# Performance work log

Hardware: AMD Instinct MI355X
Metric: run time of the kernel (lower is better)

## Reference

```python
import jax, jax.numpy as jnp
import numpy as np

QMAX = 7.0            # int4 narrow range: [-7, 7]
SCALING_MIN_VAL = 2e-16


def fake_quant_weight_per_channel(w):
    """Brevitas CommonIntWeightPerChannelQuant, bit_width=4.

    Per-output-channel float scale from abs-max stats, narrow-range signed
    int4 round+clamp, then dequantize. STE so gradients pass through.
    w: [O, I, KH, KW]
    """
    amax = jnp.max(jnp.abs(w), axis=(1, 2, 3), keepdims=True)   # [O,1,1,1]
    scale = jnp.maximum(amax / QMAX, SCALING_MIN_VAL)
    wq = jnp.clip(jnp.round(w / scale), -QMAX, QMAX) * scale
    # straight-through estimator (matches Brevitas round_ste backward)
    return w + jax.lax.stop_gradient(wq - w)


def setup_inputs() -> dict:
    key = jax.random.key(0)
    kx, kw = jax.random.split(key)
    x = jax.random.normal(kx, (32, 256, 56, 56), dtype=jnp.float32)
    # conv weight [out_channels, in_channels, kh, kw]
    w = jax.random.normal(kw, (256, 256, 3, 3), dtype=jnp.float32) * 0.05
    return {"x": x, "w": w}


def reference(x, w):
    wq = fake_quant_weight_per_channel(w)
    return jax.lax.conv_general_dilated(
        x, wq,
        window_strides=(1, 1),
        padding=((1, 1), (1, 1)),
        dimension_numbers=("NCHW", "OIHW", "NCHW"),
    )
```

## Files before the change

kernel.cpp:

```cpp
#include <hip/hip_runtime.h>
#include <cstdint>
#include <cstddef>

typedef __bf16 bf16x8 __attribute__((ext_vector_type(8)));
typedef float  f32x16 __attribute__((ext_vector_type(16)));
typedef int    i32x4  __attribute__((ext_vector_type(4)));

#define QMAX 7.0f
#define SCALE_MIN 2e-16f

#define BAR()     asm volatile("s_barrier" ::: "memory")
#define WAITVM(N) asm volatile("s_waitcnt vmcnt(" #N ")" ::: "memory")

__global__ __launch_bounds__(256) void quant_w_kernel(const float* __restrict__ w,
                                                      __bf16* __restrict__ wq) {
    const int o = blockIdx.x;
    const int t = threadIdx.x;
    const float* wo = w + (size_t)o * 2304;

    float vals[9];
    float m = 0.f;
    #pragma unroll
    for (int i = 0; i < 9; ++i) {
        float v = wo[t + i * 256];
        vals[i] = v;
        m = fmaxf(m, fabsf(v));
    }
    #pragma unroll
    for (int off = 32; off >= 1; off >>= 1) m = fmaxf(m, __shfl_down(m, off));
    __shared__ float red[4];
    __shared__ float s_scale;
    if ((t & 63) == 0) red[t >> 6] = m;
    __syncthreads();
    if (t == 0) {
        float am = fmaxf(fmaxf(red[0], red[1]), fmaxf(red[2], red[3]));
        s_scale = fmaxf(am / QMAX, SCALE_MIN);
    }
    __syncthreads();
    const float scale = s_scale;

    #pragma unroll
    for (int i = 0; i < 9; ++i) {
        int idx = t + i * 256;
        int c = idx / 9;
        int tap = idx - c * 9;
        float q = rintf(vals[i] / scale);
        q = fminf(QMAX, fmaxf(-QMAX, q));
        wq[(size_t)tap * 65536 + (size_t)o * 256 + c] = (__bf16)(q * scale);
    }
}

__global__ __launch_bounds__(256) void convert_x_kernel(const float* __restrict__ x,
                                                        __bf16* __restrict__ xpad) {
    __shared__ float tile[32][33];
    const int n  = blockIdx.z;
    const int c0 = blockIdx.y * 32;
    const int p0 = blockIdx.x * 32;
    const int tx = threadIdx.x & 31;
    const int ty = threadIdx.x >> 5;

    #pragma unroll
    for (int r = 0; r < 4; ++r) {
        int c = c0 + ty + r * 8;
        tile[ty + r * 8][tx] = x[((size_t)(n * 256 + c)) * 3136 + p0 + tx];
    }
    __syncthreads();
    #pragma unroll
    for (int r = 0; r < 4; ++r) {
        int p = p0 + ty + r * 8;
        int h = p / 56, wcol = p - h * 56;
        xpad[(((size_t)n * 58 + h + 1) * 58 + (wcol + 1)) * 256 + c0 + tx] =
            (__bf16)tile[tx][ty + r * 8];
    }
}

__global__ __launch_bounds__(256) void zero_halo_kernel(__bf16* __restrict__ xpad) {
    const int t = blockIdx.x * 256 + threadIdx.x;
    const int cvec = t & 31;
    const int r    = t >> 5;
    const int n    = r / 228;
    const int pos  = r - n * 228;
    if (n >= 32) return;
    int h, wcol;
    if      (pos < 58)  { h = 0;          wcol = pos; }
    else if (pos < 116) { h = 57;         wcol = pos - 58; }
    else if (pos < 172) { h = pos - 115;  wcol = 0; }
    else                { h = pos - 171;  wcol = 57; }
    i32x4* dst = (i32x4*)(xpad + (((size_t)n * 58 + h) * 58 + wcol) * 256);
    dst[cvec] = (i32x4){0, 0, 0, 0};
}

__device__ __forceinline__ void gload_lds16(const void* g, void* l) {
    __builtin_amdgcn_global_load_lds((const __attribute__((address_space(1))) void*)g,
                                     (__attribute__((address_space(3))) void*)l,
                                     16, 0, 0);
}

__global__ __launch_bounds__(256, 2) void conv_mfma_kernel(const __bf16* __restrict__ xpad,
                                                           const __bf16* __restrict__ wq,
                                                           float* __restrict__ out) {
    extern __shared__ __align__(16) char lds[];
    const int tid  = threadIdx.x;
    const int wv   = tid >> 6;
    const int lane = tid & 63;
    const int bid  = blockIdx.x;
    const int swz  = (bid & 7) * 98 + (bid >> 3);
    const int p0   = swz * 128;

    const int wm = wv >> 1;
    const int wn = wv & 1;

    const int trow   = tid >> 2;
    const int schunk = (tid & 3) ^ ((tid >> 4) & 3);
    const __bf16* pA[4];
    #pragma unroll
    for (int j = 0; j < 4; ++j)
        pA[j] = wq + (size_t)(j * 64 + trow) * 256 + schunk * 8;
    const __bf16* pBs[2];
    #pragma unroll
    for (int j = 0; j < 2; ++j) {
        int pos = p0 + j * 64 + trow;
        int ni = pos / 3136;
        int hw = pos - ni * 3136;
        int h = hw / 56, w = hw - h * 56;
        pBs[j] = xpad + (((size_t)ni * 58 + h) * 58 + w) * 256 + schunk * 8;
    }
    const int adst = wv * 1024;
    const int bdst = 16384 + wv * 1024;

    const int l31 = lane & 31;
    const int lk  = lane >> 5;
    const int rsw = (lane >> 2) & 3;
    int kx[2];
    #pragma unroll
    for (int ks = 0; ks < 2; ++ks)
        kx[ks] = ((ks * 2 + lk) ^ rsw) * 16;
    int arow[4], brow[2];
    #pragma unroll
    for (int m = 0; m < 4; ++m) arow[m] = (wm * 128 + m * 32 + l31) * 64;
    #pragma unroll
    for (int n = 0; n < 2; ++n) brow[n] = 16384 + (wn * 64 + n * 32 + l31) * 64;

    f32x16 acc[4][2];
    #pragma unroll
    for (int m = 0; m < 4; ++m)
        #pragma unroll
        for (int n = 0; n < 2; ++n)
            acc[m][n] = (f32x16)(0.f);

    #define STAGE(STEP, BUF)                                                  \
        {                                                                     \
            const int tap_ = (STEP) >> 3, cc_ = (STEP) & 7;                   \
            const int kh_ = tap_ / 3, kw_ = tap_ - kh_ * 3;                   \
            const size_t aoff_ = (size_t)tap_ * 65536 + cc_ * 32;             \
            const size_t boff_ = (size_t)(kh_ * 58 + kw_) * 256 + cc_ * 32;   \
            gload_lds16(pA[0] + aoff_, (BUF) + adst);                         \
            gload_lds16(pA[1] + aoff_, (BUF) + adst + 4096);                  \
            gload_lds16(pA[2] + aoff_, (BUF) + adst + 8192);                  \
            gload_lds16(pA[3] + aoff_, (BUF) + adst + 12288);                 \
            gload_lds16(pBs[0] + boff_, (BUF) + bdst);                        \
            gload_lds16(pBs[1] + boff_, (BUF) + bdst + 4096);                 \
        }

    STAGE(0, lds);
    STAGE(1, lds + 24576);

    int co = 0;
    #pragma unroll 1
    for (int s = 0; s < 72; ++s) {
        if (s < 71) { WAITVM(6); } else { WAITVM(0); }
        BAR();
        int so = co + 49152; if (so >= 73728) so -= 73728;
        if (s < 70) STAGE(s + 2, lds + so);

        const char* B = lds + co;
        bf16x8 a[4][2], b[2][2];
        #pragma unroll
        for (int m = 0; m < 4; ++m)
            #pragma unroll
            for (int ks = 0; ks < 2; ++ks)
                a[m][ks] = *(const bf16x8*)(B + arow[m] + kx[ks]);
        #pragma unroll
        for (int n = 0; n < 2; ++n)
            #pragma unroll
            for (int ks = 0; ks < 2; ++ks)
                b[n][ks] = *(const bf16x8*)(B + brow[n] + kx[ks]);

        __builtin_amdgcn_s_setprio(1);
        #pragma unroll
        for (int ks = 0; ks < 2; ++ks)
            #pragma unroll
            for (int m = 0; m < 4; ++m)
                #pragma unroll
                for (int n = 0; n < 2; ++n)
                    acc[m][n] = __builtin_amdgcn_mfma_f32_32x32x16_bf16(
                        a[m][ks], b[n][ks], acc[m][n], 0, 0, 0);
        __builtin_amdgcn_s_setprio(0);

        co += 24576; if (co == 73728) co = 0;
    }
    #undef STAGE

    const int hi = lane >> 5;
    #pragma unroll
    for (int n = 0; n < 2; ++n) {
        const int pos = p0 + wn * 64 + n * 32 + l31;
        const int ni = pos / 3136;
        const int hw = pos - ni * 3136;
        float* ob = out + (size_t)ni * 802816 + hw;
        #pragma unroll
        for (int m = 0; m < 4; ++m) {
            const int om = wm * 128 + m * 32 + 4 * hi;
            #pragma unroll
            for (int r = 0; r < 16; ++r) {
                const int o = om + (r & 3) + 8 * (r >> 2);
                ob[(size_t)o * 3136] = acc[m][n][r];
            }
        }
    }
}

__global__ __launch_bounds__(256) void conv_naive_kernel(const float* __restrict__ x,
                                                         const float* __restrict__ w,
                                                         float* __restrict__ out) {
    const int n = blockIdx.z;
    const int o = blockIdx.y;
    const int strip = blockIdx.x;
    __shared__ float wqs[2304];
    __shared__ float red[4];
    __shared__ float s_scale;
    const float* wo = w + (size_t)o * 2304;
    float m = 0.f;
    for (int i = threadIdx.x; i < 2304; i += 256) m = fmaxf(m, fabsf(wo[i]));
    #pragma unroll
    for (int off = 32; off >= 1; off >>= 1) m = fmaxf(m, __shfl_down(m, off));
    if ((threadIdx.x & 63) == 0) red[threadIdx.x >> 6] = m;
    __syncthreads();
    if (threadIdx.x == 0) {
        float am = fmaxf(fmaxf(red[0], red[1]), fmaxf(red[2], red[3]));
        s_scale = fmaxf(am / QMAX, SCALE_MIN);
    }
    __syncthreads();
    const float scale = s_scale;
    for (int i = threadIdx.x; i < 2304; i += 256) {
        float q = rintf(wo[i] / scale);
        q = fminf(QMAX, fmaxf(-QMAX, q));
        wqs[i] = q * scale;
    }
    __syncthreads();
    int p = strip * 256 + threadIdx.x;
    if (p >= 3136) return;
    int h = p / 56, wcol = p - h * 56;
    float acc = 0.f;
    for (int c = 0; c < 256; ++c) {
        const float* xc = x + ((size_t)(n * 256 + c)) * 3136;
        const float* wk = wqs + c * 9;
        #pragma unroll
        for (int kh = 0; kh < 3; ++kh) {
            int hh = h + kh - 1;
            if (hh < 0 || hh > 55) continue;
            #pragma unroll
            for (int kw = 0; kw < 3; ++kw) {
                int ww2 = wcol + kw - 1;
                if (ww2 < 0 || ww2 > 55) continue;
                acc += xc[hh * 56 + ww2] * wk[kh * 3 + kw];
            }
        }
    }
    out[((size_t)(n * 256 + o)) * 3136 + p] = acc;
}

extern "C" void kernel_launch(void* const* d_in, const int* in_sizes, int n_in,
                              void* d_out, int out_size, void* d_ws, size_t ws_size,
                              hipStream_t stream) {
    const float* x = (const float*)d_in[0];
    const float* w = (const float*)d_in[1];
    float* out = (float*)d_out;

    const size_t WQ_BYTES   = 9ull * 256 * 256 * 2;
    const size_t XPAD_OFF   = WQ_BYTES;
    const size_t XPAD_BYTES = 32ull * 58 * 58 * 256 * 2;

    if (ws_size >= XPAD_OFF + XPAD_BYTES) {
        __bf16* wq   = (__bf16*)d_ws;
        __bf16* xpad = (__bf16*)((char*)d_ws + XPAD_OFF);
        hipFuncSetAttribute((const void*)conv_mfma_kernel,
                            hipFuncAttributeMaxDynamicSharedMemorySize, 73728);
        zero_halo_kernel<<<912, 256, 0, stream>>>(xpad);
        quant_w_kernel<<<256, 256, 0, stream>>>(w, wq);
        convert_x_kernel<<<dim3(98, 8, 32), 256, 0, stream>>>(x, xpad);
        conv_mfma_kernel<<<784, 256, 73728, stream>>>(xpad, wq, out);
    } else {
        conv_naive_kernel<<<dim3(13, 256, 32), 256, 0, stream>>>(x, w, out);
    }
}
```

Baseline: 181.9 us.

## Make conv kernel persistent with atomic tile scheduler and split-K LDS loads

Turns the MFMA conv kernel into a persistent kernel launched with 512 blocks. Each block repeatedly claims a 128-position output tile through an atomic ticket counter, which is reset with a memset before launch. The main loop now issues each prefetch before waiting, keeping one stage in flight instead of two. It also splits each stage's LDS reads and MFMAs into two halves separated by extra barriers, and drops the XCD-aware block swizzle. The aim is to remove the tail imbalance of 784 tiles over the CUs and shorten the LDS-to-MFMA dependency, at the cost of extra barriers, less prefetch depth, and atomic and memset overhead.

```diff
diff --git a/kernel.cpp b/kernel.cpp
--- a/kernel.cpp
+++ b/kernel.cpp
@@ -98,14 +98,13 @@
 
 __global__ __launch_bounds__(256, 2) void conv_mfma_kernel(const __bf16* __restrict__ xpad,
                                                            const __bf16* __restrict__ wq,
-                                                           float* __restrict__ out) {
+                                                           float* __restrict__ out,
+                                                           int* __restrict__ ticket) {
     extern __shared__ __align__(16) char lds[];
+    int* s_t = (int*)(lds + 73728);
     const int tid  = threadIdx.x;
     const int wv   = tid >> 6;
     const int lane = tid & 63;
-    const int bid  = blockIdx.x;
-    const int swz  = (bid & 7) * 98 + (bid >> 3);
-    const int p0   = swz * 128;
 
     const int wm = wv >> 1;
     const int wn = wv & 1;
@@ -116,15 +115,6 @@
     #pragma unroll
     for (int j = 0; j < 4; ++j)
         pA[j] = wq + (size_t)(j * 64 + trow) * 256 + schunk * 8;
-    const __bf16* pBs[2];
-    #pragma unroll
-    for (int j = 0; j < 2; ++j) {
-        int pos = p0 + j * 64 + trow;
-        int ni = pos / 3136;
-        int hw = pos - ni * 3136;
-        int h = hw / 56, w = hw - h * 56;
-        pBs[j] = xpad + (((size_t)ni * 58 + h) * 58 + w) * 256 + schunk * 8;
-    }
     const int adst = wv * 1024;
     const int bdst = 16384 + wv * 1024;
 
@@ -140,81 +130,114 @@
     for (int m = 0; m < 4; ++m) arow[m] = (wm * 128 + m * 32 + l31) * 64;
     #pragma unroll
     for (int n = 0; n < 2; ++n) brow[n] = 16384 + (wn * 64 + n * 32 + l31) * 64;
-
-    f32x16 acc[4][2];
-    #pragma unroll
-    for (int m = 0; m < 4; ++m)
+    const int hi = lane >> 5;
+
+    for (;;) {
+        __syncthreads();
+        if (tid == 0) *s_t = atomicAdd(ticket, 1);
+        __syncthreads();
+        const int tile = *s_t;
+        if (tile >= 784) break;
+        const int p0 = tile * 128;
+
+        const __bf16* pBs[2];
         #pragma unroll
-        for (int n = 0; n < 2; ++n)
-            acc[m][n] = (f32x16)(0.f);
-
-    #define STAGE(STEP, BUF)                                                  \
-        {                                                                     \
-            const int tap_ = (STEP) >> 3, cc_ = (STEP) & 7;                   \
-            const int kh_ = tap_ / 3, kw_ = tap_ - kh_ * 3;                   \
-            const size_t aoff_ = (size_t)tap_ * 65536 + cc_ * 32;             \
-            const size_t boff_ = (size_t)(kh_ * 58 + kw_) * 256 + cc_ * 32;   \
-            gload_lds16(pA[0] + aoff_, (BUF) + adst);                         \
-            gload_lds16(pA[1] + aoff_, (BUF) + adst + 4096);                  \
-            gload_lds16(pA[2] + aoff_, (BUF) + adst + 8192);                  \
-            gload_lds16(pA[3] + aoff_, (BUF) + adst + 12288);                 \
-            gload_lds16(pBs[0] + boff_, (BUF) + bdst);                        \
-            gload_lds16(pBs[1] + boff_, (BUF) + bdst + 4096);                 \
+        for (int j = 0; j < 2; ++j) {
+            int pos = p0 + j * 64 + trow;
+            int ni = pos / 3136;
+            int hw = pos - ni * 3136;
+            int h = hw / 56, w = hw - h * 56;
+            pBs[j] = xpad + (((size_t)ni * 58 + h) * 58 + w) * 256 + schunk * 8;
         }
 
-    STAGE(0, lds);
-    STAGE(1, lds + 24576);
-
-    int co = 0;
-    #pragma unroll 1
-    for (int s = 0; s < 72; ++s) {
-        if (s < 71) { WAITVM(6); } else { WAITVM(0); }
-        BAR();
-        int so = co + 49152; if (so >= 73728) so -= 73728;
-        if (s < 70) STAGE(s + 2, lds + so);
-
-        const char* B = lds + co;
-        bf16x8 a[4][2], b[2][2];
+        f32x16 acc[4][2];
         #pragma unroll
         for (int m = 0; m < 4; ++m)
             #pragma unroll
-            for (int ks = 0; ks < 2; ++ks)
-                a[m][ks] = *(const bf16x8*)(B + arow[m] + kx[ks]);
-        #pragma unroll
-        for (int n = 0; n < 2; ++n)
-            #pragma unroll
-            for (int ks = 0; ks < 2; ++ks)
-                b[n][ks] = *(const bf16x8*)(B + brow[n] + kx[ks]);
-
-        __builtin_amdgcn_s_setprio(1);
-        #pragma unroll
-        for (int ks = 0; ks < 2; ++ks)
+            for (int n = 0; n < 2; ++n)
+                acc[m][n] = (f32x16)(0.f);
+
+        #define STAGE(STEP, BUF)                                                  \
+            {                                                                     \
+                const int tap_ = (STEP) >> 3, cc_ = (STEP) & 7;                   \
+                const int kh_ = tap_ / 3, kw_ = tap_ - kh_ * 3;                   \
+                const size_t aoff_ = (size_t)tap_ * 65536 + cc_ * 32;             \
+                const size_t boff_ = (size_t)(kh_ * 58 + kw_) * 256 + cc_ * 32;   \
+                gload_lds16(pA[0] + aoff_, (BUF) + adst);                         \
+                gload_lds16(pA[1] + aoff_, (BUF) + adst + 4096);                  \
+                gload_lds16(pA[2] + aoff_, (BUF) + adst + 8192);                  \
+                gload_lds16(pA[3] + aoff_, (BUF) + adst + 12288);                 \
+                gload_lds16(pBs[0] + boff_, (BUF) + bdst);                        \
+                gload_lds16(pBs[1] + boff_, (BUF) + bdst + 4096);                 \
+            }
+
+        STAGE(0, lds);
+
+        int co = 0;
+        #pragma unroll 1
+        for (int s = 0; s < 72; ++s) {
+            int no = co + 24576; if (no == 73728) no = 0;
+            if (s < 71) {
+                STAGE(s + 1, lds + no);
+                WAITVM(6);
+            } else {
+                WAITVM(0);
+            }
+            BAR();
+            const char* B = lds + co;
+
+            bf16x8 a0_[4], b0_[2];
+            #pragma unroll
+            for (int m = 0; m < 4; ++m)
+                a0_[m] = *(const bf16x8*)(B + arow[m] + kx[0]);
+            #pragma unroll
+            for (int n = 0; n < 2; ++n)
+                b0_[n] = *(const bf16x8*)(B + brow[n] + kx[0]);
+            BAR();
+            __builtin_amdgcn_s_setprio(1);
             #pragma unroll
             for (int m = 0; m < 4; ++m)
                 #pragma unroll
                 for (int n = 0; n < 2; ++n)
                     acc[m][n] = __builtin_amdgcn_mfma_f32_32x32x16_bf16(
-                        a[m][ks], b[n][ks], acc[m][n], 0, 0, 0);
-        __builtin_amdgcn_s_setprio(0);
-
-        co += 24576; if (co == 73728) co = 0;
-    }
-    #undef STAGE
-
-    const int hi = lane >> 5;
-    #pragma unroll
-    for (int n = 0; n < 2; ++n) {
-        const int pos = p0 + wn * 64 + n * 32 + l31;
-        const int ni = pos / 3136;
-        const int hw = pos - ni * 3136;
-        float* ob = out + (size_t)ni * 802816 + hw;
+                        a0_[m], b0_[n], acc[m][n], 0, 0, 0);
+            __builtin_amdgcn_s_setprio(0);
+
+            bf16x8 a1_[4], b1_[2];
+            #pragma unroll
+            for (int m = 0; m < 4; ++m)
+                a1_[m] = *(const bf16x8*)(B + arow[m] + kx[1]);
+            #pragma unroll
+            for (int n = 0; n < 2; ++n)
+                b1_[n] = *(const bf16x8*)(B + brow[n] + kx[1]);
+            BAR();
+            __builtin_amdgcn_s_setprio(1);
+            #pragma unroll
+            for (int m = 0; m < 4; ++m)
+                #pragma unroll
+                for (int n = 0; n < 2; ++n)
+                    acc[m][n] = __builtin_amdgcn_mfma_f32_32x32x16_bf16(
+                        a1_[m], b1_[n], acc[m][n], 0, 0, 0);
+            __builtin_amdgcn_s_setprio(0);
+
+            co = no;
+        }
+        #undef STAGE
+
         #pragma unroll
-        for (int m = 0; m < 4; ++m) {
-            const int om = wm * 128 + m * 32 + 4 * hi;
-            #pragma unroll
-            for (int r = 0; r < 16; ++r) {
-                const int o = om + (r & 3) + 8 * (r >> 2);
-                ob[(size_t)o * 3136] = acc[m][n][r];
+        for (int n = 0; n < 2; ++n) {
+            const int pos = p0 + wn * 64 + n * 32 + l31;
+            const int ni = pos / 3136;
+            const int hw = pos - ni * 3136;
+            float* ob = out + (size_t)ni * 802816 + hw;
+            #pragma unroll
+            for (int m = 0; m < 4; ++m) {
+                const int om = wm * 128 + m * 32 + 4 * hi;
+                #pragma unroll
+                for (int r = 0; r < 16; ++r) {
+                    const int o = om + (r & 3) + 8 * (r >> 2);
+                    ob[(size_t)o * 3136] = acc[m][n][r];
+                }
             }
         }
     }
@@ -280,16 +303,19 @@
     const size_t WQ_BYTES   = 9ull * 256 * 256 * 2;
     const size_t XPAD_OFF   = WQ_BYTES;
     const size_t XPAD_BYTES = 32ull * 58 * 58 * 256 * 2;
-
-    if (ws_size >= XPAD_OFF + XPAD_BYTES) {
+    const size_t TICKET_OFF = XPAD_OFF + XPAD_BYTES;
+
+    if (ws_size >= TICKET_OFF + 64) {
         __bf16* wq   = (__bf16*)d_ws;
         __bf16* xpad = (__bf16*)((char*)d_ws + XPAD_OFF);
+        int* ticket  = (int*)((char*)d_ws + TICKET_OFF);
         hipFuncSetAttribute((const void*)conv_mfma_kernel,
-                            hipFuncAttributeMaxDynamicSharedMemorySize, 73728);
+                            hipFuncAttributeMaxDynamicSharedMemorySize, 73792);
+        hipMemsetAsync(ticket, 0, 4, stream);
         zero_halo_kernel<<<912, 256, 0, stream>>>(xpad);
         quant_w_kernel<<<256, 256, 0, stream>>>(w, wq);
         convert_x_kernel<<<dim3(98, 8, 32), 256, 0, stream>>>(x, xpad);
-        conv_mfma_kernel<<<784, 256, 73728, stream>>>(xpad, wq, out);
+        conv_mfma_kernel<<<512, 256, 73792, stream>>>(xpad, wq, out, ticket);
     } else {
         conv_naive_kernel<<<dim3(13, 256, 32), 256, 0, stream>>>(x, w, out);
     }
```

New measurement: 182.7 us. About the same (+0.4%).
